# Kernel tuning notes

Measured on AMD Instinct MI355X. Metric: run time of the kernel, lower is better.

Reference implementation:

```python
import jax
import jax.numpy as jnp
import numpy as np

N = 256   # hardcoded in the torch module via expand(256, 256)
D = 256
K = 16
M_MARGIN = 0.6
T_THRESH = 0.0025
EPS = 1e-12


def setup_inputs() -> dict:
    key = jax.random.key(0)
    k1, k2 = jax.random.split(key)
    yi = jax.random.normal(k1, (N, D), dtype=jnp.float32)
    yi_t = jax.random.normal(k2, (N, D), dtype=jnp.float32)
    return {"yi": yi, "yi_t": yi_t}


def _l2_normalize(x):
    return x / jnp.sqrt(jnp.sum(x * x, axis=-1, keepdims=True) + EPS)


def reference(yi, yi_t):
    yi_n = _l2_normalize(yi)      # [N, D]
    yit_n = _l2_normalize(yi_t)   # [N, D]

    # pairwise half-distances: [N, N]
    diff = yi_n[:, None, :] - yi_n[None, :, :]           # [N, N, D]
    dis_yii = 0.5 * jnp.sqrt(jnp.sum(diff * diff, axis=-1) + EPS)

    # K+1 smallest distances per row (self is smallest)
    neg_vals, topk_idx = jax.lax.top_k(-dis_yii, K + 1)  # [N, K+1]
    nbr_idx = topk_idx[:, 1:]                            # [N, K] exclude self

    yj = yi_n[nbr_idx]                                   # [N, K, D]
    dis_yij = 0.5 * jnp.sqrt(jnp.sum((yi_n[:, None, :] - yj) ** 2, axis=-1) + EPS)
    dis_yi_tj = 0.5 * jnp.sqrt(jnp.sum((yit_n[:, None, :] - yj) ** 2, axis=-1) + EPS)

    e1 = jnp.sum((dis_yij - dis_yi_tj) ** 2 - T_THRESH)

    # margin term: dist(yi, yi_t) + m - (second smallest pairwise dist)
    dis_yi_yi_t = 0.5 * jnp.sqrt(jnp.sum((yi_n - yit_n) ** 2, axis=-1) + EPS)  # [N]
    second_nn = -neg_vals[:, 1]                          # [N]
    out = dis_yi_yi_t + M_MARGIN - second_nn
    e2 = jnp.sum(jnp.maximum(out, 0.0))

    return e1 + e2
```

## Files before the change

kernel.cpp:

```cpp
#include <hip/hip_runtime.h>
#include <math.h>

#define NN 256
#define DD 256
#define KK 16
#define M_MARGIN 0.6f
#define T_THRESH 0.0025f
#define EPS 1e-12f

__global__ void __launch_bounds__(512) blcd_fused_kernel(
    const float* __restrict__ yi, const float* __restrict__ yit,
    float* __restrict__ out)
{
    __shared__ float s_yi[DD];
    __shared__ float s_yit[DD];
    __shared__ float sdis[NN];
    __shared__ float red[24];

    const int i = blockIdx.x;
    const int t = threadIdx.x;
    const int j = t >> 1;
    const int h = t & 1;

    float a = 0.0f, b = 0.0f;
    if (t < DD) {
        a = yi [i * DD + t];
        b = yit[i * DD + t];
        s_yi[t]  = a;
        s_yit[t] = b;
    }
    float r0 = a * a, r1 = b * b, r2 = a * b;
    #pragma unroll
    for (int off = 32; off > 0; off >>= 1) {
        r0 += __shfl_down(r0, off, 64);
        r1 += __shfl_down(r1, off, 64);
        r2 += __shfl_down(r2, off, 64);
    }
    const int w = t >> 6;
    if ((t & 63) == 0) { red[w] = r0; red[8 + w] = r1; red[16 + w] = r2; }
    __syncthreads();

    const float nn_i  = ((red[0]  + red[1])  + (red[2]  + red[3]))
                      + ((red[4]  + red[5])  + (red[6]  + red[7]));
    const float nn_it = ((red[8]  + red[9])  + (red[10] + red[11]))
                      + ((red[12] + red[13]) + (red[14] + red[15]));
    const float cross = ((red[16] + red[17]) + (red[18] + red[19]))
                      + ((red[20] + red[21]) + (red[22] + red[23]));
    const float inv_ni  = 1.0f / sqrtf(nn_i  + EPS);
    const float inv_nit = 1.0f / sqrtf(nn_it + EPS);

    const float4* __restrict__ rj  = (const float4*)(yi + j * DD);
    const float4* __restrict__ si  = (const float4*)s_yi;
    const float4* __restrict__ sit = (const float4*)s_yit;
    float4 q4  = make_float4(0.f, 0.f, 0.f, 0.f);
    float4 qt4 = make_float4(0.f, 0.f, 0.f, 0.f);
    float4 nn4 = make_float4(0.f, 0.f, 0.f, 0.f);
    #pragma unroll 8
    for (int k = 0; k < DD / 8; ++k) {
        const int d4 = 2 * k + h;
        float4 y = rj[d4];
        float4 u = si[d4];
        float4 v = sit[d4];
        q4.x  += y.x * u.x; q4.y  += y.y * u.y; q4.z  += y.z * u.z; q4.w  += y.w * u.w;
        qt4.x += y.x * v.x; qt4.y += y.y * v.y; qt4.z += y.z * v.z; qt4.w += y.w * v.w;
        nn4.x += y.x * y.x; nn4.y += y.y * y.y; nn4.z += y.z * y.z; nn4.w += y.w * y.w;
    }
    float q  = (q4.x  + q4.y ) + (q4.z  + q4.w );
    float qt = (qt4.x + qt4.y) + (qt4.z + qt4.w);
    float nn = (nn4.x + nn4.y) + (nn4.z + nn4.w);
    q  += __shfl_xor(q,  1, 64);
    qt += __shfl_xor(qt, 1, 64);
    nn += __shfl_xor(nn, 1, 64);

    const float inv_nt = 1.0f / sqrtf(nn + EPS);
    const float c    = q  * inv_nt * inv_ni;
    const float ct   = qt * inv_nt * inv_nit;
    const float myv  = 0.5f * sqrtf(fmaxf(2.0f - 2.0f * c , 0.0f) + EPS);
    const float myvt = 0.5f * sqrtf(fmaxf(2.0f - 2.0f * ct, 0.0f) + EPS);
    if (h == 0) sdis[j] = myv;
    __syncthreads();

    int rank = 0;
    const float4* sd4 = (const float4*)sdis;
    #pragma unroll 8
    for (int k = h * (NN / 8); k < (h + 1) * (NN / 8); ++k) {
        float4 v = sd4[k];
        const int jj = k * 4;
        rank += (v.x < myv || (v.x == myv && (jj + 0) < j)) ? 1 : 0;
        rank += (v.y < myv || (v.y == myv && (jj + 1) < j)) ? 1 : 0;
        rank += (v.z < myv || (v.z == myv && (jj + 2) < j)) ? 1 : 0;
        rank += (v.w < myv || (v.w == myv && (jj + 3) < j)) ? 1 : 0;
    }
    rank += __shfl_xor(rank, 1, 64);

    float contrib = 0.0f;
    if (h == 0) {
        if (rank >= 1 && rank <= KK) {
            const float dd = myv - myvt;
            contrib = dd * dd - T_THRESH;
        }
        if (rank == 1) {
            const float cc = cross * inv_ni * inv_nit;
            const float d_iit = 0.5f * sqrtf(fmaxf(2.0f - 2.0f * cc, 0.0f) + EPS);
            contrib += fmaxf(d_iit + M_MARGIN - myv, 0.0f);
        }
    }

    #pragma unroll
    for (int off = 32; off > 0; off >>= 1) contrib += __shfl_down(contrib, off, 64);
    __syncthreads();
    if ((t & 63) == 0) red[w] = contrib;
    __syncthreads();
    if (t == 0)
        atomicAdd(out, ((red[0] + red[1]) + (red[2] + red[3]))
                     + ((red[4] + red[5]) + (red[6] + red[7])));
}

extern "C" void kernel_launch(void* const* d_in, const int* in_sizes, int n_in,
                              void* d_out, int out_size, void* d_ws, size_t ws_size,
                              hipStream_t stream) {
    (void)in_sizes; (void)n_in; (void)out_size; (void)d_ws; (void)ws_size;

    const float* yi  = (const float*)d_in[0];
    const float* yit = (const float*)d_in[1];
    float* out = (float*)d_out;

    hipMemsetAsync(out, 0, sizeof(float), stream);
    blcd_fused_kernel<<<NN, 512, 0, stream>>>(yi, yit, out);
}
```

Before: 71.48 us.

## Precompute row inverse norms in a prep kernel instead of per-pair recomputation

Adds a small prep kernel that computes inverse L2 norms for yi and yi_t, the yi-to-yi_t distance, and zeroes the output, storing them in workspace. The main kernel reads these instead of recomputing the norm of each neighbour row inside the dot-product loop, which removes a third of the FMAs per pair and the block reduction for the i-row norms. The hipMemsetAsync is replaced by the prep kernel's write. This adds a second kernel launch and a dependency through global memory.

```diff
diff --git a/kernel.cpp b/kernel.cpp
--- a/kernel.cpp
+++ b/kernel.cpp
@@ -8,53 +8,66 @@
 #define T_THRESH 0.0025f
 #define EPS 1e-12f
 
-__global__ void __launch_bounds__(512) blcd_fused_kernel(
+__global__ void __launch_bounds__(256) prep_kernel(
     const float* __restrict__ yi, const float* __restrict__ yit,
-    float* __restrict__ out)
+    float* __restrict__ invn, float* __restrict__ invnt,
+    float* __restrict__ diit, float* __restrict__ out)
+{
+    const int t    = threadIdx.x;
+    const int lane = t & 63;
+    const int row  = blockIdx.x * 4 + (t >> 6);
+
+    const float4 a = ((const float4*)(yi  + row * DD))[lane];
+    const float4 b = ((const float4*)(yit + row * DD))[lane];
+    float r0 = (a.x * a.x + a.y * a.y) + (a.z * a.z + a.w * a.w);
+    float r1 = (b.x * b.x + b.y * b.y) + (b.z * b.z + b.w * b.w);
+    float r2 = (a.x * b.x + a.y * b.y) + (a.z * b.z + a.w * b.w);
+    #pragma unroll
+    for (int off = 32; off > 0; off >>= 1) {
+        r0 += __shfl_down(r0, off, 64);
+        r1 += __shfl_down(r1, off, 64);
+        r2 += __shfl_down(r2, off, 64);
+    }
+    if (lane == 0) {
+        const float iny  = 1.0f / sqrtf(r0 + EPS);
+        const float inyt = 1.0f / sqrtf(r1 + EPS);
+        invn [row] = iny;
+        invnt[row] = inyt;
+        const float c = r2 * iny * inyt;
+        diit [row] = 0.5f * sqrtf(fmaxf(2.0f - 2.0f * c, 0.0f) + EPS);
+    }
+    if (blockIdx.x == 0 && t == 0) out[0] = 0.0f;
+}
+
+__global__ void __launch_bounds__(512) blcd_main_kernel(
+    const float* __restrict__ yi, const float* __restrict__ yit,
+    const float* __restrict__ invn, const float* __restrict__ invnt,
+    const float* __restrict__ diit, float* __restrict__ out)
 {
     __shared__ float s_yi[DD];
     __shared__ float s_yit[DD];
     __shared__ float sdis[NN];
-    __shared__ float red[24];
+    __shared__ float red[8];
 
     const int i = blockIdx.x;
     const int t = threadIdx.x;
     const int j = t >> 1;
     const int h = t & 1;
 
-    float a = 0.0f, b = 0.0f;
     if (t < DD) {
-        a = yi [i * DD + t];
-        b = yit[i * DD + t];
-        s_yi[t]  = a;
-        s_yit[t] = b;
+        s_yi [t] = yi [i * DD + t];
+        s_yit[t] = yit[i * DD + t];
     }
-    float r0 = a * a, r1 = b * b, r2 = a * b;
-    #pragma unroll
-    for (int off = 32; off > 0; off >>= 1) {
-        r0 += __shfl_down(r0, off, 64);
-        r1 += __shfl_down(r1, off, 64);
-        r2 += __shfl_down(r2, off, 64);
-    }
-    const int w = t >> 6;
-    if ((t & 63) == 0) { red[w] = r0; red[8 + w] = r1; red[16 + w] = r2; }
+    const float inv_ni  = invn [i];
+    const float inv_nit = invnt[i];
+    const float inv_nj  = invn [j];
     __syncthreads();
-
-    const float nn_i  = ((red[0]  + red[1])  + (red[2]  + red[3]))
-                      + ((red[4]  + red[5])  + (red[6]  + red[7]));
-    const float nn_it = ((red[8]  + red[9])  + (red[10] + red[11]))
-                      + ((red[12] + red[13]) + (red[14] + red[15]));
-    const float cross = ((red[16] + red[17]) + (red[18] + red[19]))
-                      + ((red[20] + red[21]) + (red[22] + red[23]));
-    const float inv_ni  = 1.0f / sqrtf(nn_i  + EPS);
-    const float inv_nit = 1.0f / sqrtf(nn_it + EPS);
 
     const float4* __restrict__ rj  = (const float4*)(yi + j * DD);
     const float4* __restrict__ si  = (const float4*)s_yi;
     const float4* __restrict__ sit = (const float4*)s_yit;
     float4 q4  = make_float4(0.f, 0.f, 0.f, 0.f);
     float4 qt4 = make_float4(0.f, 0.f, 0.f, 0.f);
-    float4 nn4 = make_float4(0.f, 0.f, 0.f, 0.f);
     #pragma unroll 8
     for (int k = 0; k < DD / 8; ++k) {
         const int d4 = 2 * k + h;
@@ -63,18 +76,14 @@
         float4 v = sit[d4];
         q4.x  += y.x * u.x; q4.y  += y.y * u.y; q4.z  += y.z * u.z; q4.w  += y.w * u.w;
         qt4.x += y.x * v.x; qt4.y += y.y * v.y; qt4.z += y.z * v.z; qt4.w += y.w * v.w;
-        nn4.x += y.x * y.x; nn4.y += y.y * y.y; nn4.z += y.z * y.z; nn4.w += y.w * y.w;
     }
     float q  = (q4.x  + q4.y ) + (q4.z  + q4.w );
     float qt = (qt4.x + qt4.y) + (qt4.z + qt4.w);
-    float nn = (nn4.x + nn4.y) + (nn4.z + nn4.w);
     q  += __shfl_xor(q,  1, 64);
     qt += __shfl_xor(qt, 1, 64);
-    nn += __shfl_xor(nn, 1, 64);
 
-    const float inv_nt = 1.0f / sqrtf(nn + EPS);
-    const float c    = q  * inv_nt * inv_ni;
-    const float ct   = qt * inv_nt * inv_nit;
+    const float c    = q  * inv_nj * inv_ni;
+    const float ct   = qt * inv_nj * inv_nit;
     const float myv  = 0.5f * sqrtf(fmaxf(2.0f - 2.0f * c , 0.0f) + EPS);
     const float myvt = 0.5f * sqrtf(fmaxf(2.0f - 2.0f * ct, 0.0f) + EPS);
     if (h == 0) sdis[j] = myv;
@@ -100,16 +109,13 @@
             contrib = dd * dd - T_THRESH;
         }
         if (rank == 1) {
-            const float cc = cross * inv_ni * inv_nit;
-            const float d_iit = 0.5f * sqrtf(fmaxf(2.0f - 2.0f * cc, 0.0f) + EPS);
-            contrib += fmaxf(d_iit + M_MARGIN - myv, 0.0f);
+            contrib += fmaxf(diit[i] + M_MARGIN - myv, 0.0f);
         }
     }
 
     #pragma unroll
     for (int off = 32; off > 0; off >>= 1) contrib += __shfl_down(contrib, off, 64);
-    __syncthreads();
-    if ((t & 63) == 0) red[w] = contrib;
+    if ((t & 63) == 0) red[t >> 6] = contrib;
     __syncthreads();
     if (t == 0)
         atomicAdd(out, ((red[0] + red[1]) + (red[2] + red[3]))
@@ -119,12 +125,16 @@
 extern "C" void kernel_launch(void* const* d_in, const int* in_sizes, int n_in,
                               void* d_out, int out_size, void* d_ws, size_t ws_size,
                               hipStream_t stream) {
-    (void)in_sizes; (void)n_in; (void)out_size; (void)d_ws; (void)ws_size;
+    (void)in_sizes; (void)n_in; (void)out_size; (void)ws_size;
 
     const float* yi  = (const float*)d_in[0];
     const float* yit = (const float*)d_in[1];
     float* out = (float*)d_out;
 
-    hipMemsetAsync(out, 0, sizeof(float), stream);
-    blcd_fused_kernel<<<NN, 512, 0, stream>>>(yi, yit, out);
+    float* invn  = (float*)d_ws;
+    float* invnt = invn  + NN;
+    float* diit  = invnt + NN;
+
+    prep_kernel<<<NN / 4, 256, 0, stream>>>(yi, yit, invn, invnt, diit, out);
+    blcd_main_kernel<<<NN, 512, 0, stream>>>(yi, yit, invn, invnt, diit, out);
 }
```

Result: no change. 72.05 us (+0.8%).
